# Optimization experiments

Measured on AMD Instinct MI355X. Metric: run time of the kernel, lower is better.

## Reference

```python
import jax, jax.numpy as jnp
import numpy as np

HEADS = 16
HEAD_DIM = 64
QUAD_C = 5.0   # 2quad: exp(x) ~ (x + c)^2
EPS = 1e-6


def setup_inputs() -> dict:
    key = jax.random.key(0)
    k1, k2, k3 = jax.random.split(key, 3)
    B, T, H = 2, 2048, 1024
    x = jax.random.normal(k1, (B, T, H), dtype=jnp.float32)
    # scaled init to keep pre-activation scores sane
    Wqkv = jax.random.normal(k2, (H, 3 * H), dtype=jnp.float32) * (H ** -0.5)
    Wo = jax.random.normal(k3, (H, H), dtype=jnp.float32) * (H ** -0.5)
    tau = jnp.full((HEADS,), 5.0, dtype=jnp.float32)
    return {"x": x, "Wqkv": Wqkv, "Wo": Wo, "tau": tau}


def reference(x, Wqkv, Wo, tau):
    B, T, C = x.shape
    h, d = HEADS, HEAD_DIM
    qkv = x @ Wqkv                                  # [B,T,3C]
    q, k, v = jnp.split(qkv, 3, axis=-1)
    q = q.reshape(B, T, h, d).transpose(0, 2, 1, 3)  # [B,h,T,d]
    k = k.reshape(B, T, h, d).transpose(0, 2, 1, 3)
    v = v.reshape(B, T, h, d).transpose(0, 2, 1, 3)
    # tau-scaled scores
    s = jnp.einsum("bhqd,bhkd->bhqk", q, k) / (jnp.sqrt(jnp.float32(d)) * tau[None, :, None, None])
    # 2quad attention: (s + c)^2 normalized over keys (non-softmax)
    e = jnp.square(s + QUAD_C)                       # [B,h,T,T], >=0
    w = e / (jnp.sum(e, axis=-1, keepdims=True) + EPS)
    out = jnp.einsum("bhqk,bhkd->bhqd", w, v)        # [B,h,T,d]
    out = out.transpose(0, 2, 1, 3).reshape(B, T, C)
    return out @ Wo
```

## Files before the change

kernel.cpp:

```cpp
#include <hip/hip_runtime.h>
#include <hip/hip_bf16.h>


typedef unsigned short ushort_t;
typedef __attribute__((ext_vector_type(8))) short short8;
typedef __attribute__((ext_vector_type(4))) float f32x4;

#define B_      2
#define T_      2048
#define C_      1024
#define HEADS_  16
#define D_      64
#define M_      (B_ * T_)
#define N3_     (3 * C_)

__device__ __forceinline__ ushort_t f2bf(float f) {
  __hip_bfloat16 h = __float2bfloat16(f);
  return *reinterpret_cast<ushort_t*>(&h);
}

__global__ __launch_bounds__(256) void cast_x_kernel(const float* __restrict__ x,
                                                     ushort_t* __restrict__ xb) {
  int i = blockIdx.x * 256 + threadIdx.x;
  float4 f = ((const float4*)x)[i];
  ushort_t* o = xb + (size_t)i * 4;
  o[0] = f2bf(f.x); o[1] = f2bf(f.y); o[2] = f2bf(f.z); o[3] = f2bf(f.w);
}

__global__ __launch_bounds__(256) void transpose_cast_w(const float* __restrict__ in,
                                                        ushort_t* __restrict__ out,
                                                        int R, int Cc) {
  __shared__ float tile[64][65];
  int rb = blockIdx.y, cb = blockIdx.x;
  int c = threadIdx.x & 63;
  int r0 = threadIdx.x >> 6;
#pragma unroll
  for (int i = 0; i < 16; ++i) {
    int r = r0 + i * 4;
    tile[r][c] = in[(size_t)(rb * 64 + r) * Cc + cb * 64 + c];
  }
  __syncthreads();
#pragma unroll
  for (int i = 0; i < 16; ++i) {
    int r = r0 + i * 4;
    out[(size_t)(cb * 64 + r) * R + rb * 64 + c] = f2bf(tile[c][r]);
  }
}

__global__ __launch_bounds__(256) void transpose_v_kernel(const ushort_t* __restrict__ v,
                                                          ushort_t* __restrict__ vT) {
  __shared__ ushort_t tile[64][72];
  int bh = blockIdx.y, tb = blockIdx.x;
  int c = threadIdx.x & 63;
  int r0 = threadIdx.x >> 6;
#pragma unroll
  for (int i = 0; i < 16; ++i) {
    int r = r0 + i * 4;
    tile[r][c] = v[((size_t)bh * T_ + tb * 64 + r) * D_ + c];
  }
  __syncthreads();
#pragma unroll
  for (int i = 0; i < 16; ++i) {
    int r = r0 + i * 4;
    vT[((size_t)bh * D_ + r) * T_ + tb * 64 + c] = tile[c][r];
  }
}

__device__ __forceinline__ void gemm_tile(const ushort_t* __restrict__ A,
                                          const ushort_t* __restrict__ Bt,
                                          int K, int tm, int tn,
                                          ushort_t* lds, f32x4 acc[4][4]) {
  const int tid = threadIdx.x;
  const int lane = tid & 63, wave = tid >> 6;
  const int wm = wave >> 1, wn = wave & 1;
  const int lr = lane & 15, lk = lane >> 4;
  ushort_t* As = lds;
  ushort_t* Bs = lds + 128 * 72;
  const ushort_t* Ag = A + (size_t)tm * 128 * K;
  const ushort_t* Bg = Bt + (size_t)tn * 128 * K;

  for (int kt = 0; kt < K; kt += 64) {
#pragma unroll
    for (int i = 0; i < 4; ++i) {
      int cch = tid + i * 256; int row = cch >> 3, kc = cch & 7;
      *(short8*)&As[row * 72 + kc * 8] =
          *(const short8*)&Ag[(size_t)row * K + kt + kc * 8];
    }
#pragma unroll
    for (int i = 0; i < 4; ++i) {
      int cch = tid + i * 256; int row = cch >> 3, kc = cch & 7;
      *(short8*)&Bs[row * 72 + kc * 8] =
          *(const short8*)&Bg[(size_t)row * K + kt + kc * 8];
    }
    __syncthreads();
#pragma unroll
    for (int kk = 0; kk < 64; kk += 32) {
      short8 a[4], b[4];
#pragma unroll
      for (int m = 0; m < 4; ++m)
        a[m] = *(const short8*)&As[(wm * 64 + m * 16 + lr) * 72 + kk + lk * 8];
#pragma unroll
      for (int n = 0; n < 4; ++n)
        b[n] = *(const short8*)&Bs[(wn * 64 + n * 16 + lr) * 72 + kk + lk * 8];
#pragma unroll
      for (int m = 0; m < 4; ++m)
#pragma unroll
        for (int n = 0; n < 4; ++n)
          acc[m][n] = __builtin_amdgcn_mfma_f32_16x16x32_bf16(a[m], b[n], acc[m][n], 0, 0, 0);
    }
    __syncthreads();
  }
}

__global__ __launch_bounds__(256) void gemm_qkv(const ushort_t* __restrict__ xb,
                                                const ushort_t* __restrict__ wT,
                                                ushort_t* __restrict__ qg,
                                                ushort_t* __restrict__ kg,
                                                ushort_t* __restrict__ vg) {
  __shared__ __align__(16) ushort_t lds[2 * 128 * 72];
  f32x4 acc[4][4];
#pragma unroll
  for (int m = 0; m < 4; ++m)
#pragma unroll
    for (int n = 0; n < 4; ++n) acc[m][n] = (f32x4){0.f, 0.f, 0.f, 0.f};

  gemm_tile(xb, wT, C_, blockIdx.y, blockIdx.x, lds, acc);

  const int lane = threadIdx.x & 63, wave = threadIdx.x >> 6;
  const int wm = wave >> 1, wn = wave & 1;
  const int lr = lane & 15, lk = lane >> 4;
#pragma unroll
  for (int m = 0; m < 4; ++m)
#pragma unroll
    for (int n = 0; n < 4; ++n)
#pragma unroll
      for (int r = 0; r < 4; ++r) {
        int row = blockIdx.y * 128 + wm * 64 + m * 16 + lk * 4 + r;
        int col = blockIdx.x * 128 + wn * 64 + n * 16 + lr;
        int b = row >> 11, t = row & 2047;
        int part = col >> 10, idx = col & 1023;
        int h = idx >> 6, j = idx & 63;
        ushort_t* dst = (part == 0) ? qg : (part == 1) ? kg : vg;
        dst[(((size_t)(b * HEADS_ + h)) * T_ + t) * D_ + j] = f2bf(acc[m][n][r]);
      }
}

__global__ __launch_bounds__(256) void gemm_out(const ushort_t* __restrict__ ab,
                                                const ushort_t* __restrict__ woT,
                                                float* __restrict__ out) {
  __shared__ __align__(16) ushort_t lds[2 * 128 * 72];
  f32x4 acc[4][4];
#pragma unroll
  for (int m = 0; m < 4; ++m)
#pragma unroll
    for (int n = 0; n < 4; ++n) acc[m][n] = (f32x4){0.f, 0.f, 0.f, 0.f};

  gemm_tile(ab, woT, C_, blockIdx.y, blockIdx.x, lds, acc);

  const int lane = threadIdx.x & 63, wave = threadIdx.x >> 6;
  const int wm = wave >> 1, wn = wave & 1;
  const int lr = lane & 15, lk = lane >> 4;
#pragma unroll
  for (int m = 0; m < 4; ++m)
#pragma unroll
    for (int n = 0; n < 4; ++n)
#pragma unroll
      for (int r = 0; r < 4; ++r) {
        int row = blockIdx.y * 128 + wm * 64 + m * 16 + lk * 4 + r;
        int col = blockIdx.x * 128 + wn * 64 + n * 16 + lr;
        out[(size_t)row * C_ + col] = acc[m][n][r];
      }
}

__global__ __launch_bounds__(256) void attn_kernel(const ushort_t* __restrict__ qg,
                                                   const ushort_t* __restrict__ kg,
                                                   const ushort_t* __restrict__ vTg,
                                                   const float* __restrict__ tau,
                                                   ushort_t* __restrict__ attn_out) {
  __shared__ __align__(16) ushort_t Ks[64 * 72];
  __shared__ __align__(16) ushort_t Vts[64 * 72];
  __shared__ __align__(16) ushort_t Es[4][16 * 72];

  const int tid = threadIdx.x, lane = tid & 63, w = tid >> 6;
  const int lr = lane & 15, lk = lane >> 4;
  const int qt = blockIdx.x, bh = blockIdx.y;
  const int b = bh >> 4, h = bh & 15;
  const float inv = 1.0f / (8.0f * tau[h]);

  const ushort_t* qb = qg + ((size_t)bh * T_ + qt * 64 + w * 16) * D_;
  const ushort_t* kb = kg + (size_t)bh * T_ * D_;
  const ushort_t* vb = vTg + (size_t)bh * D_ * T_;

  short8 qa[2];
#pragma unroll
  for (int ks = 0; ks < 2; ++ks)
    qa[ks] = *(const short8*)&qb[lr * D_ + ks * 32 + lk * 8];

  f32x4 acc[4];
  float denomp[4];
#pragma unroll
  for (int n = 0; n < 4; ++n) acc[n] = (f32x4){0.f, 0.f, 0.f, 0.f};
#pragma unroll
  for (int r = 0; r < 4; ++r) denomp[r] = 0.f;

  for (int kv = 0; kv < T_; kv += 64) {
#pragma unroll
    for (int i = 0; i < 2; ++i) {
      int cch = tid + i * 256; int row = cch >> 3, kc = cch & 7;
      *(short8*)&Ks[row * 72 + kc * 8] =
          *(const short8*)&kb[(size_t)(kv + row) * D_ + kc * 8];
      *(short8*)&Vts[row * 72 + kc * 8] =
          *(const short8*)&vb[(size_t)row * T_ + kv + kc * 8];
    }
    __syncthreads();

    f32x4 s[4];
#pragma unroll
    for (int n = 0; n < 4; ++n) s[n] = (f32x4){0.f, 0.f, 0.f, 0.f};
#pragma unroll
    for (int kk = 0; kk < 2; ++kk) {
      short8 bk[4];
#pragma unroll
      for (int n = 0; n < 4; ++n)
        bk[n] = *(const short8*)&Ks[(n * 16 + lr) * 72 + kk * 32 + lk * 8];
#pragma unroll
      for (int n = 0; n < 4; ++n)
        s[n] = __builtin_amdgcn_mfma_f32_16x16x32_bf16(qa[kk], bk[n], s[n], 0, 0, 0);
    }

#pragma unroll
    for (int n = 0; n < 4; ++n)
#pragma unroll
      for (int r = 0; r < 4; ++r) {
        float t = fmaf(s[n][r], inv, 5.0f);
        float e = t * t;
        denomp[r] += e;
        Es[w][(lk * 4 + r) * 72 + n * 16 + lr] = f2bf(e);
      }

#pragma unroll
    for (int kk = 0; kk < 2; ++kk) {
      short8 ea, vv[4];
      ea = *(const short8*)&Es[w][lr * 72 + kk * 32 + lk * 8];
#pragma unroll
      for (int n = 0; n < 4; ++n)
        vv[n] = *(const short8*)&Vts[(n * 16 + lr) * 72 + kk * 32 + lk * 8];
#pragma unroll
      for (int n = 0; n < 4; ++n)
        acc[n] = __builtin_amdgcn_mfma_f32_16x16x32_bf16(ea, vv[n], acc[n], 0, 0, 0);
    }
    __syncthreads();
  }

#pragma unroll
  for (int r = 0; r < 4; ++r) {
    float v = denomp[r];
    v += __shfl_xor(v, 1); v += __shfl_xor(v, 2);
    v += __shfl_xor(v, 4); v += __shfl_xor(v, 8);
    denomp[r] = v;
  }

#pragma unroll
  for (int n = 0; n < 4; ++n)
#pragma unroll
    for (int r = 0; r < 4; ++r) {
      int qrow = qt * 64 + w * 16 + lk * 4 + r;
      int d = n * 16 + lr;
      float o = acc[n][r] / (denomp[r] + 1e-6f);
      attn_out[((size_t)(b * T_ + qrow)) * C_ + h * D_ + d] = f2bf(o);
    }
}

extern "C" void kernel_launch(void* const* d_in, const int* in_sizes, int n_in,
                              void* d_out, int out_size, void* d_ws, size_t ws_size,
                              hipStream_t stream) {
  const float* x    = (const float*)d_in[0];
  const float* Wqkv = (const float*)d_in[1];
  const float* Wo   = (const float*)d_in[2];
  const float* tau  = (const float*)d_in[3];
  float* out = (float*)d_out;

  char* ws = (char*)d_ws;
  ushort_t* xb    = (ushort_t*)(ws);
  ushort_t* wqkvT = (ushort_t*)(ws + 8388608);
  ushort_t* woT   = (ushort_t*)(ws + 14680064);
  ushort_t* qg    = (ushort_t*)(ws + 16777216);
  ushort_t* kg    = (ushort_t*)(ws + 25165824);
  ushort_t* ab    = (ushort_t*)(ws + 33554432);
  ushort_t* vg  = (ushort_t*)d_out;
  ushort_t* vTg = (ushort_t*)d_out + 4194304;

  cast_x_kernel<<<4096, 256, 0, stream>>>(x, xb);
  transpose_cast_w<<<dim3(48, 16), 256, 0, stream>>>(Wqkv, wqkvT, 1024, 3072);
  transpose_cast_w<<<dim3(16, 16), 256, 0, stream>>>(Wo, woT, 1024, 1024);
  gemm_qkv<<<dim3(24, 32), 256, 0, stream>>>(xb, wqkvT, qg, kg, vg);
  transpose_v_kernel<<<dim3(32, 32), 256, 0, stream>>>(vg, vTg);
  attn_kernel<<<dim3(32, 32), 256, 0, stream>>>(qg, kg, vTg, tau, ab);
  gemm_out<<<dim3(8, 32), 256, 0, stream>>>(ab, woT, out);
}
```

Baseline: 155.8 us.

## Rewrite attention with 32x32 MFMA, register-resident E fragments, split-K waves

The attention kernel now uses 32x32x16 bf16 MFMAs and computes S transposed (K·Qᵀ), so the squared scores can be packed with cvt_pk_bf16 and shuffled with permlane32_swap straight into A-operand fragments. This removes the LDS round trip for the E matrix. Each block now covers 128 queries with 128 keys per step, splitting keys across wave pairs and reducing partial outputs and denominators through LDS at the end. The aim is fewer LDS accesses, more work per MFMA and more K/V reuse, at the cost of a larger register footprint, half as many blocks, and an extra reduction pass.

```diff
diff --git a/kernel.cpp b/kernel.cpp
--- a/kernel.cpp
+++ b/kernel.cpp
@@ -5,18 +5,36 @@
 typedef unsigned short ushort_t;
 typedef __attribute__((ext_vector_type(8))) short short8;
 typedef __attribute__((ext_vector_type(4))) float f32x4;
+typedef __attribute__((ext_vector_type(16))) float f32x16;
 
 #define B_      2
 #define T_      2048
 #define C_      1024
 #define HEADS_  16
 #define D_      64
-#define M_      (B_ * T_)
-#define N3_     (3 * C_)
+
+union frag_u { unsigned u[4]; short8 s8; };
 
 __device__ __forceinline__ ushort_t f2bf(float f) {
   __hip_bfloat16 h = __float2bfloat16(f);
   return *reinterpret_cast<ushort_t*>(&h);
+}
+
+__device__ __forceinline__ unsigned cvt_pk_bf16(float lo, float hi) {
+  unsigned r;
+  asm("v_cvt_pk_bf16_f32 %0, %1, %2" : "=v"(r) : "v"(lo), "v"(hi));
+  return r;
+}
+
+__device__ __forceinline__ void permlane32_swap(unsigned &a, unsigned &b) {
+  asm volatile("v_permlane32_swap_b32 %0, %1" : "+v"(a), "+v"(b));
+}
+
+__device__ __forceinline__ f32x16 zero16() {
+  f32x16 z;
+#pragma unroll
+  for (int i = 0; i < 16; ++i) z[i] = 0.f;
+  return z;
 }
 
 __global__ __launch_bounds__(256) void cast_x_kernel(const float* __restrict__ x,
@@ -172,103 +190,139 @@
       }
 }
 
-__global__ __launch_bounds__(256) void attn_kernel(const ushort_t* __restrict__ qg,
-                                                   const ushort_t* __restrict__ kg,
-                                                   const ushort_t* __restrict__ vTg,
-                                                   const float* __restrict__ tau,
-                                                   ushort_t* __restrict__ attn_out) {
-  __shared__ __align__(16) ushort_t Ks[64 * 72];
-  __shared__ __align__(16) ushort_t Vts[64 * 72];
-  __shared__ __align__(16) ushort_t Es[4][16 * 72];
-
-  const int tid = threadIdx.x, lane = tid & 63, w = tid >> 6;
-  const int lr = lane & 15, lk = lane >> 4;
+__global__ __launch_bounds__(256, 2) void attn_kernel(const ushort_t* __restrict__ qg,
+                                                      const ushort_t* __restrict__ kg,
+                                                      const ushort_t* __restrict__ vTg,
+                                                      const float* __restrict__ tau,
+                                                      ushort_t* __restrict__ attn_out) {
+  __shared__ __align__(16) ushort_t kvbuf[128 * 72 + 64 * 136];
+  __shared__ float denom_lds[2][2][2][32];
+  ushort_t* Ks  = kvbuf;
+  ushort_t* Vts = kvbuf + 128 * 72;
+
+  const int tid = threadIdx.x, lane = tid & 63;
+  const int w = tid >> 6, wq = w >> 1, wk = w & 1;
+  const int l31 = lane & 31, hi = lane >> 5, hi8 = hi * 8;
   const int qt = blockIdx.x, bh = blockIdx.y;
   const int b = bh >> 4, h = bh & 15;
   const float inv = 1.0f / (8.0f * tau[h]);
 
-  const ushort_t* qb = qg + ((size_t)bh * T_ + qt * 64 + w * 16) * D_;
-  const ushort_t* kb = kg + (size_t)bh * T_ * D_;
-  const ushort_t* vb = vTg + (size_t)bh * D_ * T_;
-
-  short8 qa[2];
-#pragma unroll
-  for (int ks = 0; ks < 2; ++ks)
-    qa[ks] = *(const short8*)&qb[lr * D_ + ks * 32 + lk * 8];
-
-  f32x4 acc[4];
-  float denomp[4];
-#pragma unroll
-  for (int n = 0; n < 4; ++n) acc[n] = (f32x4){0.f, 0.f, 0.f, 0.f};
-#pragma unroll
-  for (int r = 0; r < 4; ++r) denomp[r] = 0.f;
-
-  for (int kv = 0; kv < T_; kv += 64) {
-#pragma unroll
-    for (int i = 0; i < 2; ++i) {
-      int cch = tid + i * 256; int row = cch >> 3, kc = cch & 7;
+  const ushort_t* kb_ = kg  + (size_t)bh * T_ * D_;
+  const ushort_t* vb_ = vTg + (size_t)bh * D_ * T_;
+  const ushort_t* qp  = qg  + ((size_t)bh * T_ + qt * 128 + wq * 64) * D_;
+
+  short8 qf[2][4];
+#pragma unroll
+  for (int qb = 0; qb < 2; ++qb)
+#pragma unroll
+    for (int dc = 0; dc < 4; ++dc)
+      qf[qb][dc] = *(const short8*)&qp[(qb * 32 + l31) * D_ + dc * 16 + hi8];
+
+  f32x16 acc[2][2];
+  acc[0][0] = zero16(); acc[0][1] = zero16();
+  acc[1][0] = zero16(); acc[1][1] = zero16();
+  float denomp[2] = {0.f, 0.f};
+
+  for (int rnd = 0; rnd < T_ / 128; ++rnd) {
+    const int kv0 = rnd * 128;
+#pragma unroll
+    for (int i = 0; i < 4; ++i) {
+      int cch = tid + i * 256;
+      int row = cch >> 3, kc = cch & 7;
       *(short8*)&Ks[row * 72 + kc * 8] =
-          *(const short8*)&kb[(size_t)(kv + row) * D_ + kc * 8];
-      *(short8*)&Vts[row * 72 + kc * 8] =
-          *(const short8*)&vb[(size_t)row * T_ + kv + kc * 8];
+          *(const short8*)&kb_[(size_t)(kv0 + row) * D_ + kc * 8];
+    }
+#pragma unroll
+    for (int i = 0; i < 4; ++i) {
+      int cch = tid + i * 256;
+      int row = cch >> 4, kc = cch & 15;
+      *(short8*)&Vts[row * 136 + kc * 8] =
+          *(const short8*)&vb_[(size_t)row * T_ + kv0 + kc * 8];
     }
     __syncthreads();
 
-    f32x4 s[4];
-#pragma unroll
-    for (int n = 0; n < 4; ++n) s[n] = (f32x4){0.f, 0.f, 0.f, 0.f};
-#pragma unroll
-    for (int kk = 0; kk < 2; ++kk) {
-      short8 bk[4];
-#pragma unroll
-      for (int n = 0; n < 4; ++n)
-        bk[n] = *(const short8*)&Ks[(n * 16 + lr) * 72 + kk * 32 + lk * 8];
-#pragma unroll
-      for (int n = 0; n < 4; ++n)
-        s[n] = __builtin_amdgcn_mfma_f32_16x16x32_bf16(qa[kk], bk[n], s[n], 0, 0, 0);
-    }
-
-#pragma unroll
-    for (int n = 0; n < 4; ++n)
-#pragma unroll
-      for (int r = 0; r < 4; ++r) {
-        float t = fmaf(s[n][r], inv, 5.0f);
-        float e = t * t;
-        denomp[r] += e;
-        Es[w][(lk * 4 + r) * 72 + n * 16 + lr] = f2bf(e);
-      }
-
-#pragma unroll
-    for (int kk = 0; kk < 2; ++kk) {
-      short8 ea, vv[4];
-      ea = *(const short8*)&Es[w][lr * 72 + kk * 32 + lk * 8];
-#pragma unroll
-      for (int n = 0; n < 4; ++n)
-        vv[n] = *(const short8*)&Vts[(n * 16 + lr) * 72 + kk * 32 + lk * 8];
-#pragma unroll
-      for (int n = 0; n < 4; ++n)
-        acc[n] = __builtin_amdgcn_mfma_f32_16x16x32_bf16(ea, vv[n], acc[n], 0, 0, 0);
+#pragma unroll
+    for (int kb = 0; kb < 2; ++kb) {
+      const int krow0 = wk * 64 + kb * 32;
+      f32x16 s[2]; s[0] = zero16(); s[1] = zero16();
+#pragma unroll
+      for (int dc = 0; dc < 4; ++dc) {
+        short8 kf = *(const short8*)&Ks[(krow0 + l31) * 72 + dc * 16 + hi8];
+        s[0] = __builtin_amdgcn_mfma_f32_32x32x16_bf16(kf, qf[0][dc], s[0], 0, 0, 0);
+        s[1] = __builtin_amdgcn_mfma_f32_32x32x16_bf16(kf, qf[1][dc], s[1], 0, 0, 0);
+      }
+
+      frag_u ef[2][2];
+#pragma unroll
+      for (int qb = 0; qb < 2; ++qb) {
+        float ev[16];
+        float dsum = 0.f;
+#pragma unroll
+        for (int r = 0; r < 16; ++r) {
+          float t = fmaf(s[qb][r], inv, 5.0f);
+          ev[r] = t * t;
+          dsum += ev[r];
+        }
+        denomp[qb] += dsum;
+        unsigned P[8];
+#pragma unroll
+        for (int p = 0; p < 8; ++p) P[p] = cvt_pk_bf16(ev[2 * p], ev[2 * p + 1]);
+        unsigned a0 = P[0], b0 = P[2]; permlane32_swap(a0, b0);
+        unsigned a1 = P[1], b1 = P[3]; permlane32_swap(a1, b1);
+        ef[qb][0].u[0] = a0; ef[qb][0].u[1] = a1; ef[qb][0].u[2] = b0; ef[qb][0].u[3] = b1;
+        unsigned a2 = P[4], b2 = P[6]; permlane32_swap(a2, b2);
+        unsigned a3 = P[5], b3 = P[7]; permlane32_swap(a3, b3);
+        ef[qb][1].u[0] = a2; ef[qb][1].u[1] = a3; ef[qb][1].u[2] = b2; ef[qb][1].u[3] = b3;
+      }
+
+#pragma unroll
+      for (int c = 0; c < 2; ++c)
+#pragma unroll
+        for (int db = 0; db < 2; ++db) {
+          short8 vf = *(const short8*)&Vts[(db * 32 + l31) * 136 + krow0 + c * 16 + hi8];
+          acc[0][db] = __builtin_amdgcn_mfma_f32_32x32x16_bf16(ef[0][c].s8, vf, acc[0][db], 0, 0, 0);
+          acc[1][db] = __builtin_amdgcn_mfma_f32_32x32x16_bf16(ef[1][c].s8, vf, acc[1][db], 0, 0, 0);
+        }
     }
     __syncthreads();
   }
 
 #pragma unroll
-  for (int r = 0; r < 4; ++r) {
-    float v = denomp[r];
-    v += __shfl_xor(v, 1); v += __shfl_xor(v, 2);
-    v += __shfl_xor(v, 4); v += __shfl_xor(v, 8);
-    denomp[r] = v;
-  }
-
-#pragma unroll
-  for (int n = 0; n < 4; ++n)
-#pragma unroll
-    for (int r = 0; r < 4; ++r) {
-      int qrow = qt * 64 + w * 16 + lk * 4 + r;
-      int d = n * 16 + lr;
-      float o = acc[n][r] / (denomp[r] + 1e-6f);
-      attn_out[((size_t)(b * T_ + qrow)) * C_ + h * D_ + d] = f2bf(o);
-    }
+  for (int qb = 0; qb < 2; ++qb) {
+    float v = denomp[qb];
+    v += __shfl_xor(v, 32);
+    if (lane < 32) denom_lds[wk][wq][qb][l31] = v;
+  }
+  float* out_lds = (float*)kvbuf;
+  if (wk == 1) {
+#pragma unroll
+    for (int qb = 0; qb < 2; ++qb)
+#pragma unroll
+      for (int db = 0; db < 2; ++db)
+#pragma unroll
+        for (int r = 0; r < 16; ++r) {
+          int qr = qb * 32 + (r & 3) + 8 * (r >> 2) + 4 * hi;
+          out_lds[(wq * 64 + qr) * 64 + db * 32 + l31] = acc[qb][db][r];
+        }
+  }
+  __syncthreads();
+  if (wk == 0) {
+#pragma unroll
+    for (int qb = 0; qb < 2; ++qb)
+#pragma unroll
+      for (int r = 0; r < 16; ++r) {
+        int cr = (r & 3) + 8 * (r >> 2) + 4 * hi;
+        int qr = qb * 32 + cr;
+        float dt = denom_lds[0][wq][qb][cr] + denom_lds[1][wq][qb][cr];
+        float dinv = 1.0f / (dt + 1e-6f);
+#pragma unroll
+        for (int db = 0; db < 2; ++db) {
+          float val = acc[qb][db][r] + out_lds[(wq * 64 + qr) * 64 + db * 32 + l31];
+          int grow = b * T_ + qt * 128 + wq * 64 + qr;
+          attn_out[(size_t)grow * C_ + h * 64 + db * 32 + l31] = f2bf(val * dinv);
+        }
+      }
+  }
 }
 
 extern "C" void kernel_launch(void* const* d_in, const int* in_sizes, int n_in,
@@ -295,6 +349,6 @@
   transpose_cast_w<<<dim3(16, 16), 256, 0, stream>>>(Wo, woT, 1024, 1024);
   gemm_qkv<<<dim3(24, 32), 256, 0, stream>>>(xb, wqkvT, qg, kg, vg);
   transpose_v_kernel<<<dim3(32, 32), 256, 0, stream>>>(vg, vTg);
-  attn_kernel<<<dim3(32, 32), 256, 0, stream>>>(qg, kg, vTg, tau, ab);
+  attn_kernel<<<dim3(16, 32), 256, 0, stream>>>(qg, kg, vTg, tau, ab);
   gemm_out<<<dim3(8, 32), 256, 0, stream>>>(ab, woT, out);
 }
```

Result: faster. 126.1 us (-19.1%).
